# Optimization experiments

Measured on AMD Instinct MI355X. Metric: run time of the kernel, lower is better.

Reference implementation:

```python
import jax, jax.numpy as jnp
import numpy as np

LOG2 = float(np.log(2.0))

def ssp(x):
    # shifted softplus: softplus(x) - log(2)
    return jax.nn.softplus(x) - LOG2

N_NODES = 50000
N_EDGES = 600000
HID = 128
NF = 128

def setup_inputs() -> dict:
    key = jax.random.key(0)
    ks = jax.random.split(key, 10)
    x = jax.random.normal(ks[0], (N_NODES, HID), dtype=jnp.float32)
    edge_attr = jax.random.normal(ks[1], (N_EDGES, NF), dtype=jnp.float32)
    edge_index = jax.random.randint(ks[2], (2, N_EDGES), 0, N_NODES, dtype=jnp.int32)
    s = 1.0 / np.sqrt(NF)
    fc1_w = jax.random.uniform(ks[3], (NF, HID), jnp.float32, -s, s)   # CFConv.fc1 (no bias)
    f_w1 = jax.random.uniform(ks[4], (NF, NF), jnp.float32, -s, s)     # filter_mlp[0]
    f_b1 = jnp.zeros((NF,), jnp.float32)
    f_w2 = jax.random.uniform(ks[5], (NF, NF), jnp.float32, -s, s)     # filter_mlp[2]
    f_b2 = jnp.zeros((NF,), jnp.float32)
    s_w1 = jax.random.uniform(ks[6], (NF, NF), jnp.float32, -s, s)     # StateMLP.fc1
    s_w2 = jax.random.uniform(ks[7], (NF, NF), jnp.float32, -s, s)     # StateMLP.fc2
    return {"x": x, "edge_attr": edge_attr, "edge_index": edge_index,
            "fc1_w": fc1_w, "f_w1": f_w1, "f_b1": f_b1, "f_w2": f_w2,
            "f_b2": f_b2, "s_w1": s_w1, "s_w2": s_w2}

def reference(x, edge_attr, edge_index, fc1_w, f_w1, f_b1, f_w2, f_b2, s_w1, s_w2):
    src, dst = edge_index[0], edge_index[1]  # x_j = x[src], aggregate at dst
    # filter network on edge attributes: [E, NF]
    W = ssp(ssp(edge_attr @ f_w1.T + f_b1) @ f_w2.T + f_b2)
    # message: gather source nodes, linear transform, filter multiply
    msg = (x[src] @ fc1_w.T) * W                               # [E, NF]
    # scatter-add aggregation into nodes
    agg = jax.ops.segment_sum(msg, dst, num_segments=x.shape[0])  # [N, NF]
    # StateMLP
    return ssp(agg @ s_w1.T) @ s_w2.T
```

## Files before the change

### kernel.cpp

```cpp
#include <hip/hip_runtime.h>

#define F 128

typedef __attribute__((ext_vector_type(8))) __bf16 bf16x8;
typedef __attribute__((ext_vector_type(4))) float floatx4;

__device__ __forceinline__ float ssp(float x) {
    return __logf(fmaf(0.5f, __expf(x), 0.5f));
}

__global__ void prep_kernel(const float* __restrict__ fc1w,
                            const float* __restrict__ fw1,
                            const float* __restrict__ fw2,
                            const float* __restrict__ sw1,
                            const float* __restrict__ sw2,
                            __bf16* __restrict__ fc1h, __bf16* __restrict__ fc1l,
                            __bf16* __restrict__ fw1h, __bf16* __restrict__ fw2h,
                            __bf16* __restrict__ sw1h, __bf16* __restrict__ sw1l,
                            __bf16* __restrict__ sw2h, __bf16* __restrict__ sw2l)
{
    int i = blockIdx.x * blockDim.x + threadIdx.x;
    if (i >= F * F) return;
    float v; __bf16 h;
    v = fc1w[i]; h = (__bf16)v; fc1h[i] = h; fc1l[i] = (__bf16)(v - (float)h);
    v = sw1[i];  h = (__bf16)v; sw1h[i] = h; sw1l[i] = (__bf16)(v - (float)h);
    v = sw2[i];  h = (__bf16)v; sw2h[i] = h; sw2l[i] = (__bf16)(v - (float)h);
    fw1h[i] = (__bf16)fw1[i];
    fw2h[i] = (__bf16)fw2[i];
}

__global__ __launch_bounds__(256) void hist_kernel(const int* __restrict__ eidx,
                                                   int* __restrict__ cnt, int E)
{
    int i = blockIdx.x * 256 + threadIdx.x;
    if (i < E) atomicAdd(&cnt[eidx[E + i]], 1);
}

__global__ __launch_bounds__(1024) void scan1_kernel(int* __restrict__ cnt,
                                                     int* __restrict__ bsums, int N)
{
    __shared__ int sd[1024];
    const int t = threadIdx.x;
    const int i = blockIdx.x * 1024 + t;
    int v = (i < N) ? cnt[i] : 0;
    sd[t] = v;
    __syncthreads();
    for (int off = 1; off < 1024; off <<= 1) {
        int add = (t >= off) ? sd[t - off] : 0;
        __syncthreads();
        sd[t] += add;
        __syncthreads();
    }
    if (i < N) cnt[i] = sd[t] - v;
    if (t == 1023) bsums[blockIdx.x] = sd[t];
}

__global__ void scan2_kernel(int* __restrict__ bsums, int nb)
{
    if (threadIdx.x == 0 && blockIdx.x == 0) {
        int acc = 0;
        for (int j = 0; j < nb; ++j) { int c = bsums[j]; bsums[j] = acc; acc += c; }
    }
}

__global__ __launch_bounds__(1024) void scan3_kernel(int* __restrict__ cnt,
                                                     const int* __restrict__ bsums, int N)
{
    int i = blockIdx.x * 1024 + threadIdx.x;
    if (i < N) cnt[i] += bsums[blockIdx.x];
}

__global__ __launch_bounds__(256) void scatter_kernel(const int* __restrict__ eidx,
                                                      int* __restrict__ cursor,
                                                      int* __restrict__ perm,
                                                      int* __restrict__ ssrc,
                                                      int* __restrict__ sdst, int E)
{
    int i = blockIdx.x * 256 + threadIdx.x;
    if (i < E) {
        int d = eidx[E + i];
        int slot = atomicAdd(&cursor[d], 1);
        perm[slot] = i;
        ssrc[slot] = eidx[i];
        sdst[slot] = d;
    }
}

__global__ __launch_bounds__(256) void fc1_kernel(
    const float* __restrict__ x, const __bf16* __restrict__ wh,
    const __bf16* __restrict__ wl, float* __restrict__ y, int M)
{
    const int tid = threadIdx.x;
    const int wv = tid >> 6, lane = tid & 63;
    const int m16 = lane & 15, q = lane >> 4;
    const int g = wv & 1, c = wv >> 1;
    const int rowA0 = blockIdx.x * 32 + g * 16 + m16;
    const int rowA = rowA0 < M ? rowA0 : M - 1;

    floatx4 acc[4] = {};
    #pragma unroll
    for (int ks = 0; ks < 4; ++ks) {
        const int kb = ks * 32 + q * 8;
        const float4* p = (const float4*)(x + (size_t)rowA * F + kb);
        float4 a0 = p[0], a1 = p[1];
        float fv[8] = {a0.x, a0.y, a0.z, a0.w, a1.x, a1.y, a1.z, a1.w};
        bf16x8 ah, al;
        #pragma unroll
        for (int i = 0; i < 8; ++i) {
            __bf16 h = (__bf16)fv[i];
            ah[i] = h; al[i] = (__bf16)(fv[i] - (float)h);
        }
        #pragma unroll
        for (int nt = 0; nt < 4; ++nt) {
            const size_t wo = (size_t)(c * 64 + nt * 16 + m16) * F + kb;
            bf16x8 bh = *(const bf16x8*)(wh + wo);
            bf16x8 bl = *(const bf16x8*)(wl + wo);
            acc[nt] = __builtin_amdgcn_mfma_f32_16x16x32_bf16(ah, bh, acc[nt], 0, 0, 0);
            acc[nt] = __builtin_amdgcn_mfma_f32_16x16x32_bf16(al, bh, acc[nt], 0, 0, 0);
            acc[nt] = __builtin_amdgcn_mfma_f32_16x16x32_bf16(ah, bl, acc[nt], 0, 0, 0);
        }
    }
    const int rowD0 = blockIdx.x * 32 + g * 16 + q * 4;
    #pragma unroll
    for (int nt = 0; nt < 4; ++nt) {
        const int col = c * 64 + nt * 16 + m16;
        #pragma unroll
        for (int r = 0; r < 4; ++r) {
            const int row = rowD0 + r;
            if (row < M) y[(size_t)row * F + col] = acc[nt][r];
        }
    }
}

__global__ __launch_bounds__(256) void edge_kernel(
    const float* __restrict__ edge_attr,
    const int* __restrict__ perm,
    const int* __restrict__ ssrc,
    const int* __restrict__ sdst,
    const float* __restrict__ fb1, const float* __restrict__ fb2,
    const __bf16* __restrict__ fw1, const __bf16* __restrict__ fw2,
    const float* __restrict__ y,
    float* __restrict__ agg, int E)
{
    __shared__ __bf16 h1[64][136];

    const int tid = threadIdx.x;
    const int wv = tid >> 6, lane = tid & 63;
    const int m16 = lane & 15, q = lane >> 4;
    const int e0 = blockIdx.x * 64;
    const int pA0 = e0 + wv * 16 + m16;
    const int pA = pA0 < E ? pA0 : E - 1;
    const int eA = perm[pA];

    floatx4 acc[8] = {};
    #pragma unroll
    for (int ks = 0; ks < 4; ++ks) {
        const int kb = ks * 32 + q * 8;
        const float4* pa = (const float4*)(edge_attr + (size_t)eA * F + kb);
        float4 a0 = pa[0], a1 = pa[1];
        float fv[8] = {a0.x, a0.y, a0.z, a0.w, a1.x, a1.y, a1.z, a1.w};
        bf16x8 aF;
        #pragma unroll
        for (int i = 0; i < 8; ++i) aF[i] = (__bf16)fv[i];
        #pragma unroll
        for (int nt = 0; nt < 8; ++nt) {
            bf16x8 bF = *(const bf16x8*)(fw1 + (size_t)(nt * 16 + m16) * F + kb);
            acc[nt] = __builtin_amdgcn_mfma_f32_16x16x32_bf16(aF, bF, acc[nt], 0, 0, 0);
        }
    }
    #pragma unroll
    for (int nt = 0; nt < 8; ++nt) {
        const int col = nt * 16 + m16;
        const float b = fb1[col];
        #pragma unroll
        for (int r = 0; r < 4; ++r) {
            const int row = wv * 16 + q * 4 + r;
            h1[row][col] = (__bf16)ssp(acc[nt][r] + b);
        }
    }
    __syncthreads();

    floatx4 zero = {};
    #pragma unroll
    for (int nt = 0; nt < 8; ++nt) acc[nt] = zero;
    #pragma unroll
    for (int ks = 0; ks < 4; ++ks) {
        const int kb = ks * 32 + q * 8;
        bf16x8 aF = *(const bf16x8*)(&h1[wv * 16 + m16][kb]);
        #pragma unroll
        for (int nt = 0; nt < 8; ++nt) {
            bf16x8 bF = *(const bf16x8*)(fw2 + (size_t)(nt * 16 + m16) * F + kb);
            acc[nt] = __builtin_amdgcn_mfma_f32_16x16x32_bf16(aF, bF, acc[nt], 0, 0, 0);
        }
    }

    int src[4], dst[4], ok[4];
    #pragma unroll
    for (int r = 0; r < 4; ++r) {
        const int p = e0 + wv * 16 + q * 4 + r;
        const int pc = p < E ? p : E - 1;
        ok[r] = (p < E);
        src[r] = ssrc[pc];
        dst[r] = sdst[pc];
    }
    #pragma unroll
    for (int nt = 0; nt < 8; ++nt) {
        const int col = nt * 16 + m16;
        const float b = fb2[col];
        float run = 0.f;
        #pragma unroll
        for (int r = 0; r < 4; ++r) {
            if (ok[r]) {
                const float wV = ssp(acc[nt][r] + b);
                run += y[(size_t)src[r] * F + col] * wV;
                const bool flush = (r == 3) || (!ok[r + 1]) || (dst[r + 1] != dst[r]);
                if (flush) {
                    unsafeAtomicAdd(&agg[(size_t)dst[r] * F + col], run);
                    run = 0.f;
                }
            }
        }
    }
}

__global__ __launch_bounds__(256) void state_kernel(
    const float* __restrict__ agg,
    const __bf16* __restrict__ w1h, const __bf16* __restrict__ w1l,
    const __bf16* __restrict__ w2h, const __bf16* __restrict__ w2l,
    float* __restrict__ out, int M)
{
    __shared__ __bf16 hh[32][136];
    __shared__ __bf16 hl[32][136];

    const int tid = threadIdx.x;
    const int wv = tid >> 6, lane = tid & 63;
    const int m16 = lane & 15, q = lane >> 4;
    const int g = wv & 1, c = wv >> 1;
    const int rowA0 = blockIdx.x * 32 + g * 16 + m16;
    const int rowA = rowA0 < M ? rowA0 : M - 1;

    floatx4 acc[4] = {};
    #pragma unroll
    for (int ks = 0; ks < 4; ++ks) {
        const int kb = ks * 32 + q * 8;
        const float4* p = (const float4*)(agg + (size_t)rowA * F + kb);
        float4 a0 = p[0], a1 = p[1];
        float fv[8] = {a0.x, a0.y, a0.z, a0.w, a1.x, a1.y, a1.z, a1.w};
        bf16x8 ah, al;
        #pragma unroll
        for (int i = 0; i < 8; ++i) {
            __bf16 h = (__bf16)fv[i];
            ah[i] = h; al[i] = (__bf16)(fv[i] - (float)h);
        }
        #pragma unroll
        for (int nt = 0; nt < 4; ++nt) {
            const size_t wo = (size_t)(c * 64 + nt * 16 + m16) * F + kb;
            bf16x8 bh = *(const bf16x8*)(w1h + wo);
            bf16x8 bl = *(const bf16x8*)(w1l + wo);
            acc[nt] = __builtin_amdgcn_mfma_f32_16x16x32_bf16(ah, bh, acc[nt], 0, 0, 0);
            acc[nt] = __builtin_amdgcn_mfma_f32_16x16x32_bf16(al, bh, acc[nt], 0, 0, 0);
            acc[nt] = __builtin_amdgcn_mfma_f32_16x16x32_bf16(ah, bl, acc[nt], 0, 0, 0);
        }
    }
    #pragma unroll
    for (int nt = 0; nt < 4; ++nt) {
        const int col = c * 64 + nt * 16 + m16;
        #pragma unroll
        for (int r = 0; r < 4; ++r) {
            const int row = g * 16 + q * 4 + r;
            const float h = ssp(acc[nt][r]);
            const __bf16 H = (__bf16)h;
            hh[row][col] = H;
            hl[row][col] = (__bf16)(h - (float)H);
        }
    }
    __syncthreads();

    floatx4 zero = {};
    #pragma unroll
    for (int nt = 0; nt < 4; ++nt) acc[nt] = zero;
    #pragma unroll
    for (int ks = 0; ks < 4; ++ks) {
        const int kb = ks * 32 + q * 8;
        bf16x8 aH = *(const bf16x8*)(&hh[g * 16 + m16][kb]);
        bf16x8 aL = *(const bf16x8*)(&hl[g * 16 + m16][kb]);
        #pragma unroll
        for (int nt = 0; nt < 4; ++nt) {
            const size_t wo = (size_t)(c * 64 + nt * 16 + m16) * F + kb;
            bf16x8 bh = *(const bf16x8*)(w2h + wo);
            bf16x8 bl = *(const bf16x8*)(w2l + wo);
            acc[nt] = __builtin_amdgcn_mfma_f32_16x16x32_bf16(aH, bh, acc[nt], 0, 0, 0);
            acc[nt] = __builtin_amdgcn_mfma_f32_16x16x32_bf16(aL, bh, acc[nt], 0, 0, 0);
            acc[nt] = __builtin_amdgcn_mfma_f32_16x16x32_bf16(aH, bl, acc[nt], 0, 0, 0);
        }
    }
    const int rowD0 = blockIdx.x * 32 + g * 16 + q * 4;
    #pragma unroll
    for (int nt = 0; nt < 4; ++nt) {
        const int col = c * 64 + nt * 16 + m16;
        #pragma unroll
        for (int r = 0; r < 4; ++r) {
            const int row = rowD0 + r;
            if (row < M) out[(size_t)row * F + col] = acc[nt][r];
        }
    }
}

extern "C" void kernel_launch(void* const* d_in, const int* in_sizes, int n_in,
                              void* d_out, int out_size, void* d_ws, size_t ws_size,
                              hipStream_t stream)
{
    const float* x         = (const float*)d_in[0];
    const float* edge_attr = (const float*)d_in[1];
    const int*   eidx      = (const int*)d_in[2];
    const float* fc1w      = (const float*)d_in[3];
    const float* fw1       = (const float*)d_in[4];
    const float* fb1       = (const float*)d_in[5];
    const float* fw2       = (const float*)d_in[6];
    const float* fb2       = (const float*)d_in[7];
    const float* sw1       = (const float*)d_in[8];
    const float* sw2       = (const float*)d_in[9];
    float* out = (float*)d_out;

    const int N = in_sizes[0] / F;
    const int E = in_sizes[1] / F;

    float* agg = (float*)d_ws;
    float* y   = agg + (size_t)N * F;
    __bf16* wb = (__bf16*)(y + (size_t)N * F);
    const int WSZ = F * F;
    __bf16* fc1h = wb;            __bf16* fc1l = wb + WSZ;
    __bf16* fw1h = wb + 2 * WSZ;  __bf16* fw2h = wb + 3 * WSZ;
    __bf16* sw1h = wb + 4 * WSZ;  __bf16* sw1l = wb + 5 * WSZ;
    __bf16* sw2h = wb + 6 * WSZ;  __bf16* sw2l = wb + 7 * WSZ;
    int* cnt   = (int*)(wb + 8 * WSZ);
    int* bsums = cnt + N;
    int* perm  = bsums + 64;
    int* ssrc  = perm + E;
    int* sdst  = ssrc + E;

    const int nb1 = (N + 1023) / 1024;

    hipMemsetAsync(agg, 0, (size_t)N * F * sizeof(float), stream);
    hipMemsetAsync(cnt, 0, (size_t)N * sizeof(int), stream);

    prep_kernel<<<(WSZ + 255) / 256, 256, 0, stream>>>(
        fc1w, fw1, fw2, sw1, sw2, fc1h, fc1l, fw1h, fw2h, sw1h, sw1l, sw2h, sw2l);

    fc1_kernel<<<(N + 31) / 32, 256, 0, stream>>>(x, fc1h, fc1l, y, N);

    hist_kernel<<<(E + 255) / 256, 256, 0, stream>>>(eidx, cnt, E);
    scan1_kernel<<<nb1, 1024, 0, stream>>>(cnt, bsums, N);
    scan2_kernel<<<1, 64, 0, stream>>>(bsums, nb1);
    scan3_kernel<<<nb1, 1024, 0, stream>>>(cnt, bsums, N);
    scatter_kernel<<<(E + 255) / 256, 256, 0, stream>>>(eidx, cnt, perm, ssrc, sdst, E);

    edge_kernel<<<(E + 63) / 64, 256, 0, stream>>>(
        edge_attr, perm, ssrc, sdst, fb1, fb2, fw1h, fw2h, y, agg, E);

    state_kernel<<<(N + 31) / 32, 256, 0, stream>>>(
        agg, sw1h, sw1l, sw2h, sw2l, out, N);
}
```

Before: 1.018 ms.

## Split edge kernel into coalesced filter pass and per-wave segmented aggregation

The fused edge kernel is split in two. A filter kernel reads edge_attr in original order, which is coalesced, computes the filter MLP, and scatters fp16 filter rows into dst-sorted slots through a pos array. A separate aggregation kernel walks the sorted edges with each wave covering 16 consecutive edges, gathers y rows and filter values, and flushes one atomic per run of equal destinations. The cnt memset is folded into prep_kernel and scan2 becomes a wave shuffle scan. This adds an E×128 fp16 intermediate round trip through memory and lowers filter precision to fp16.

```diff
diff --git a/kernel.cpp b/kernel.cpp
--- a/kernel.cpp
+++ b/kernel.cpp
@@ -1,9 +1,11 @@
 #include <hip/hip_runtime.h>
 
 #define F 128
+#define SP 16
 
 typedef __attribute__((ext_vector_type(8))) __bf16 bf16x8;
 typedef __attribute__((ext_vector_type(4))) float floatx4;
+typedef __attribute__((ext_vector_type(2))) _Float16 f16x2;
 
 __device__ __forceinline__ float ssp(float x) {
     return __logf(fmaf(0.5f, __expf(x), 0.5f));
@@ -17,9 +19,11 @@
                             __bf16* __restrict__ fc1h, __bf16* __restrict__ fc1l,
                             __bf16* __restrict__ fw1h, __bf16* __restrict__ fw2h,
                             __bf16* __restrict__ sw1h, __bf16* __restrict__ sw1l,
-                            __bf16* __restrict__ sw2h, __bf16* __restrict__ sw2l)
+                            __bf16* __restrict__ sw2h, __bf16* __restrict__ sw2l,
+                            int* __restrict__ cnt, int N)
 {
     int i = blockIdx.x * blockDim.x + threadIdx.x;
+    for (int j = i; j < N; j += gridDim.x * blockDim.x) cnt[j] = 0;
     if (i >= F * F) return;
     float v; __bf16 h;
     v = fc1w[i]; h = (__bf16)v; fc1h[i] = h; fc1l[i] = (__bf16)(v - (float)h);
@@ -57,10 +61,15 @@
 
 __global__ void scan2_kernel(int* __restrict__ bsums, int nb)
 {
-    if (threadIdx.x == 0 && blockIdx.x == 0) {
-        int acc = 0;
-        for (int j = 0; j < nb; ++j) { int c = bsums[j]; bsums[j] = acc; acc += c; }
-    }
+    const int lane = threadIdx.x & 63;
+    int v = (lane < nb) ? bsums[lane] : 0;
+    int acc = v;
+    #pragma unroll
+    for (int off = 1; off < 64; off <<= 1) {
+        int t = __shfl_up(acc, off);
+        if (lane >= off) acc += t;
+    }
+    if (lane < nb) bsums[lane] = acc - v;
 }
 
 __global__ __launch_bounds__(1024) void scan3_kernel(int* __restrict__ cnt,
@@ -72,7 +81,7 @@
 
 __global__ __launch_bounds__(256) void scatter_kernel(const int* __restrict__ eidx,
                                                       int* __restrict__ cursor,
-                                                      int* __restrict__ perm,
+                                                      int* __restrict__ pos,
                                                       int* __restrict__ ssrc,
                                                       int* __restrict__ sdst, int E)
 {
@@ -80,7 +89,7 @@
     if (i < E) {
         int d = eidx[E + i];
         int slot = atomicAdd(&cursor[d], 1);
-        perm[slot] = i;
+        pos[i] = slot;
         ssrc[slot] = eidx[i];
         sdst[slot] = d;
     }
@@ -132,31 +141,31 @@
     }
 }
 
-__global__ __launch_bounds__(256) void edge_kernel(
+__global__ __launch_bounds__(256) void filter_kernel(
     const float* __restrict__ edge_attr,
-    const int* __restrict__ perm,
-    const int* __restrict__ ssrc,
-    const int* __restrict__ sdst,
+    const int* __restrict__ pos,
     const float* __restrict__ fb1, const float* __restrict__ fb2,
     const __bf16* __restrict__ fw1, const __bf16* __restrict__ fw2,
-    const float* __restrict__ y,
-    float* __restrict__ agg, int E)
-{
-    __shared__ __bf16 h1[64][136];
+    _Float16* __restrict__ Ws, int E)
+{
+    __shared__ __align__(16) unsigned short smem[64][136];
+    __shared__ int pos_s[64];
+    __bf16 (*h1)[136] = (__bf16 (*)[136])smem;
+    _Float16 (*wo)[136] = (_Float16 (*)[136])smem;
 
     const int tid = threadIdx.x;
     const int wv = tid >> 6, lane = tid & 63;
     const int m16 = lane & 15, q = lane >> 4;
     const int e0 = blockIdx.x * 64;
-    const int pA0 = e0 + wv * 16 + m16;
-    const int pA = pA0 < E ? pA0 : E - 1;
-    const int eA = perm[pA];
+    if (tid < 64) { int e = e0 + tid; pos_s[tid] = pos[e < E ? e : E - 1]; }
+    const int rowA0 = e0 + wv * 16 + m16;
+    const int rowA = rowA0 < E ? rowA0 : E - 1;
 
     floatx4 acc[8] = {};
     #pragma unroll
     for (int ks = 0; ks < 4; ++ks) {
         const int kb = ks * 32 + q * 8;
-        const float4* pa = (const float4*)(edge_attr + (size_t)eA * F + kb);
+        const float4* pa = (const float4*)(edge_attr + (size_t)rowA * F + kb);
         float4 a0 = pa[0], a1 = pa[1];
         float fv[8] = {a0.x, a0.y, a0.z, a0.w, a1.x, a1.y, a1.z, a1.w};
         bf16x8 aF;
@@ -193,33 +202,83 @@
             acc[nt] = __builtin_amdgcn_mfma_f32_16x16x32_bf16(aF, bF, acc[nt], 0, 0, 0);
         }
     }
-
-    int src[4], dst[4], ok[4];
-    #pragma unroll
-    for (int r = 0; r < 4; ++r) {
-        const int p = e0 + wv * 16 + q * 4 + r;
-        const int pc = p < E ? p : E - 1;
-        ok[r] = (p < E);
-        src[r] = ssrc[pc];
-        dst[r] = sdst[pc];
-    }
+    __syncthreads();
+
     #pragma unroll
     for (int nt = 0; nt < 8; ++nt) {
         const int col = nt * 16 + m16;
         const float b = fb2[col];
-        float run = 0.f;
-        #pragma unroll
-        for (int r = 0; r < 4; ++r) {
-            if (ok[r]) {
-                const float wV = ssp(acc[nt][r] + b);
-                run += y[(size_t)src[r] * F + col] * wV;
-                const bool flush = (r == 3) || (!ok[r + 1]) || (dst[r + 1] != dst[r]);
-                if (flush) {
-                    unsafeAtomicAdd(&agg[(size_t)dst[r] * F + col], run);
-                    run = 0.f;
+        #pragma unroll
+        for (int r = 0; r < 4; ++r) {
+            const int row = wv * 16 + q * 4 + r;
+            wo[row][col] = (_Float16)ssp(acc[nt][r] + b);
+        }
+    }
+    __syncthreads();
+
+    #pragma unroll
+    for (int r2 = 0; r2 < 4; ++r2) {
+        const int row = wv * 16 + r2 * 4 + q;
+        const int e = e0 + row;
+        if (e < E) {
+            const uint4 v = *(const uint4*)(&wo[row][m16 * 8]);
+            *(uint4*)(Ws + (size_t)pos_s[row] * F + m16 * 8) = v;
+        }
+    }
+}
+
+__global__ __launch_bounds__(256) void agg_kernel(
+    const float* __restrict__ y, const _Float16* __restrict__ Ws,
+    const int* __restrict__ ssrc, const int* __restrict__ sdst,
+    float* __restrict__ agg, int E)
+{
+    const int tid = threadIdx.x;
+    const int wv = tid >> 6, lane = tid & 63;
+    const long s0 = ((long)blockIdx.x * 4 + wv) * SP;
+    if (s0 >= E) return;
+
+    int msrc = 0, mdst = -1;
+    if (lane < SP) {
+        long s = s0 + lane;
+        if (s < E) { msrc = ssrc[s]; mdst = sdst[s]; }
+    }
+    const int col = lane * 2;
+    float rx = 0.f, ry = 0.f;
+    int rdst = -1;
+
+    #pragma unroll
+    for (int c = 0; c < SP / 4; ++c) {
+        float2 yv[4]; float wx[4], wy[4]; int pdst[4]; bool okr[4];
+        #pragma unroll
+        for (int r = 0; r < 4; ++r) {
+            const int p = c * 4 + r;
+            const long s = s0 + p;
+            okr[r] = (s < E);
+            const int sp = __shfl(msrc, p);
+            pdst[r] = __shfl(mdst, p);
+            const long sc = okr[r] ? s : (long)(E - 1);
+            const int spc = okr[r] ? sp : 0;
+            yv[r] = *(const float2*)(y + (size_t)spc * F + col);
+            f16x2 w2 = *(const f16x2*)(Ws + (size_t)sc * F + col);
+            wx[r] = (float)w2[0]; wy[r] = (float)w2[1];
+        }
+        #pragma unroll
+        for (int r = 0; r < 4; ++r) {
+            if (!okr[r]) continue;
+            if (pdst[r] != rdst) {
+                if (rdst >= 0) {
+                    unsafeAtomicAdd(&agg[(size_t)rdst * F + col], rx);
+                    unsafeAtomicAdd(&agg[(size_t)rdst * F + col + 1], ry);
                 }
+                rx = 0.f; ry = 0.f; rdst = pdst[r];
             }
-        }
+            rx = fmaf(yv[r].x, wx[r], rx);
+            ry = fmaf(yv[r].y, wy[r], ry);
+        }
+    }
+    if (rdst >= 0) {
+        unsafeAtomicAdd(&agg[(size_t)rdst * F + col], rx);
+        unsafeAtomicAdd(&agg[(size_t)rdst * F + col + 1], ry);
     }
 }
 
@@ -333,19 +392,20 @@
     __bf16* fw1h = wb + 2 * WSZ;  __bf16* fw2h = wb + 3 * WSZ;
     __bf16* sw1h = wb + 4 * WSZ;  __bf16* sw1l = wb + 5 * WSZ;
     __bf16* sw2h = wb + 6 * WSZ;  __bf16* sw2l = wb + 7 * WSZ;
-    int* cnt   = (int*)(wb + 8 * WSZ);
+    _Float16* Ws = (_Float16*)(wb + 8 * WSZ);
+    int* cnt   = (int*)(Ws + (size_t)E * F);
     int* bsums = cnt + N;
-    int* perm  = bsums + 64;
-    int* ssrc  = perm + E;
+    int* pos   = bsums + 64;
+    int* ssrc  = pos + E;
     int* sdst  = ssrc + E;
 
     const int nb1 = (N + 1023) / 1024;
 
     hipMemsetAsync(agg, 0, (size_t)N * F * sizeof(float), stream);
-    hipMemsetAsync(cnt, 0, (size_t)N * sizeof(int), stream);
 
     prep_kernel<<<(WSZ + 255) / 256, 256, 0, stream>>>(
-        fc1w, fw1, fw2, sw1, sw2, fc1h, fc1l, fw1h, fw2h, sw1h, sw1l, sw2h, sw2l);
+        fc1w, fw1, fw2, sw1, sw2, fc1h, fc1l, fw1h, fw2h, sw1h, sw1l, sw2h, sw2l,
+        cnt, N);
 
     fc1_kernel<<<(N + 31) / 32, 256, 0, stream>>>(x, fc1h, fc1l, y, N);
 
@@ -353,10 +413,12 @@
     scan1_kernel<<<nb1, 1024, 0, stream>>>(cnt, bsums, N);
     scan2_kernel<<<1, 64, 0, stream>>>(bsums, nb1);
     scan3_kernel<<<nb1, 1024, 0, stream>>>(cnt, bsums, N);
-    scatter_kernel<<<(E + 255) / 256, 256, 0, stream>>>(eidx, cnt, perm, ssrc, sdst, E);
-
-    edge_kernel<<<(E + 63) / 64, 256, 0, stream>>>(
-        edge_attr, perm, ssrc, sdst, fb1, fb2, fw1h, fw2h, y, agg, E);
+    scatter_kernel<<<(E + 255) / 256, 256, 0, stream>>>(eidx, cnt, pos, ssrc, sdst, E);
+
+    filter_kernel<<<(E + 63) / 64, 256, 0, stream>>>(
+        edge_attr, pos, fb1, fb2, fw1h, fw2h, Ws, E);
+
+    agg_kernel<<<(E + 63) / 64, 256, 0, stream>>>(y, Ws, ssrc, sdst, agg, E);
 
     state_kernel<<<(N + 31) / 32, 256, 0, stream>>>(
         agg, sw1h, sw1l, sw2h, sw2l, out, N);
```

After: 966.4 us. 1.05x faster.
